# Optimization experiments

Measured on AMD Instinct MI355X. Metric: run time of the kernel, lower is better.

Reference implementation:

```python
import jax, jax.numpy as jnp
import numpy as np

N = 50000        # nodes
E = 600000       # edges
D_IN = 128       # node_in_channels
H = 256          # hidden_channels
G = 128          # graphs per batch
OUT = 1


def setup_inputs() -> dict:
    key = jax.random.key(0)
    ks = jax.random.split(key, 16)

    def lin(k, fan_in, fan_out):
        k1, k2 = jax.random.split(k)
        bound = 1.0 / np.sqrt(fan_in)
        W = jax.random.uniform(k1, (fan_in, fan_out), jnp.float32, -bound, bound)
        b = jax.random.uniform(k2, (fan_out,), jnp.float32, -bound, bound)
        return W, b

    x = jax.random.normal(ks[0], (N, D_IN), jnp.float32)
    edge_index = jax.random.randint(ks[1], (2, E), 0, N, jnp.int64)
    batch = jnp.sort(jax.random.randint(ks[2], (N,), 0, G, jnp.int64))

    W1, b1 = lin(ks[3], D_IN, H)   # conv1 mlp layer 1
    W2, b2 = lin(ks[4], H, H)      # conv1 mlp layer 2
    W3, b3 = lin(ks[5], H, H)      # conv2 mlp layer 1
    W4, b4 = lin(ks[6], H, H)      # conv2 mlp layer 2
    Wf1, bf1 = lin(ks[7], 2 * H, H)
    Wf2, bf2 = lin(ks[8], H, OUT)

    return {"x": x, "edge_index": edge_index, "batch": batch,
            "W1": W1, "b1": b1, "W2": W2, "b2": b2,
            "W3": W3, "b3": b3, "W4": W4, "b4": b4,
            "Wf1": Wf1, "bf1": bf1, "Wf2": Wf2, "bf2": bf2}


def _gin_conv(h, src, dst, Wa, ba, Wb, bb):
    # GINConv with eps=0: mlp(h + sum_{u->v} h[u])
    agg = jax.ops.segment_sum(h[src], dst, num_segments=h.shape[0])
    z = h + agg
    z = jax.nn.relu(z @ Wa + ba) @ Wb + bb
    return z


def reference(x, edge_index, batch,
              W1, b1, W2, b2, W3, b3, W4, b4,
              Wf1, bf1, Wf2, bf2):
    src, dst = edge_index[0], edge_index[1]

    h = jax.nn.relu(_gin_conv(x, src, dst, W1, b1, W2, b2))
    h = jax.nn.relu(_gin_conv(h, src, dst, W3, b3, W4, b4))

    # global mean / max pooling over graphs
    counts = jax.ops.segment_sum(jnp.ones((h.shape[0],), h.dtype), batch,
                                 num_segments=G)
    sums = jax.ops.segment_sum(h, batch, num_segments=G)
    mean = sums / jnp.maximum(counts, 1.0)[:, None]
    mx = jax.ops.segment_max(h, batch, num_segments=G)
    mx = jnp.where(counts[:, None] > 0, mx, 0.0)

    p = jnp.concatenate([mean, mx], axis=1)          # [G, 2H]
    out = jax.nn.relu(p @ Wf1 + bf1) @ Wf2 + bf2     # [G, OUT]
    return out
```

## Files before the change

### kernel.cpp

```cpp
#include <hip/hip_runtime.h>
#include <math.h>

#define D_IN 128
#define HDIM 256
#define PSPLIT 8

typedef __attribute__((ext_vector_type(8))) short bf16x8;
typedef __attribute__((ext_vector_type(4))) float f32x4;

__device__ inline ushort f2bf(float v) {
    union { float f; unsigned u; } c; c.f = v;
    unsigned u = c.u;
    return (ushort)((u + 0x7FFFu + ((u >> 16) & 1u)) >> 16);
}
__device__ inline float bf2f(ushort h) {
    union { unsigned u; float f; } c; c.u = ((unsigned)h) << 16; return c.f;
}
__device__ inline float bflo(unsigned u) {
    union { unsigned u; float f; } c; c.u = u << 16; return c.f;
}
__device__ inline float bfhi(unsigned u) {
    union { unsigned u; float f; } c; c.u = u & 0xFFFF0000u; return c.f;
}

__global__ __launch_bounds__(256) void zero_int_kernel(int* __restrict__ p, int n) {
    int i = blockIdx.x * 256 + threadIdx.x;
    int stride = gridDim.x * 256;
    for (; i < n; i += stride) p[i] = 0;
}

__global__ __launch_bounds__(256) void hist_kernel(
    const int* __restrict__ ei, int* __restrict__ deg, int E)
{
    int e = blockIdx.x * 256 + threadIdx.x;
    if (e < E) atomicAdd(&deg[ei[E + e]], 1);
}

__global__ __launch_bounds__(256) void scan_local_kernel(
    const int* __restrict__ deg, int* __restrict__ rowptr,
    int* __restrict__ bsum, int N)
{
    __shared__ int sh[256];
    const int t = threadIdx.x;
    const int i = blockIdx.x * 256 + t;
    int v = (i < N) ? deg[i] : 0;
    sh[t] = v;
    __syncthreads();
#pragma unroll
    for (int off = 1; off < 256; off <<= 1) {
        int x = (t >= off) ? sh[t - off] : 0;
        __syncthreads();
        sh[t] += x;
        __syncthreads();
    }
    if (i < N) rowptr[i] = sh[t] - v;
    if (t == 255) bsum[blockIdx.x] = sh[255];
}

__global__ __launch_bounds__(256) void scan_bsum_kernel(
    int* __restrict__ bsum, int* __restrict__ rowptr, int nb, int N)
{
    __shared__ int sh[256];
    const int t = threadIdx.x;
    int v = (t < nb) ? bsum[t] : 0;
    sh[t] = v;
    __syncthreads();
#pragma unroll
    for (int off = 1; off < 256; off <<= 1) {
        int x = (t >= off) ? sh[t - off] : 0;
        __syncthreads();
        sh[t] += x;
        __syncthreads();
    }
    if (t < nb) bsum[t] = sh[t] - v;
    if (t == 255) rowptr[N] = sh[255];
}

__global__ __launch_bounds__(256) void scan_apply_kernel(
    int* __restrict__ rowptr, int* __restrict__ cursor,
    const int* __restrict__ bsum, int N)
{
    int i = blockIdx.x * 256 + threadIdx.x;
    if (i < N) {
        int v = rowptr[i] + bsum[blockIdx.x];
        rowptr[i] = v;
        cursor[i] = v;
    }
}

__global__ __launch_bounds__(256) void fill_kernel(
    const int* __restrict__ ei, int* __restrict__ cursor,
    int* __restrict__ srclist, int E)
{
    int e = blockIdx.x * 256 + threadIdx.x;
    if (e < E) {
        int s = ei[e];
        int d = ei[E + e];
        int pos = atomicAdd(&cursor[d], 1);
        srclist[pos] = s;
    }
}

template<int K>
__global__ __launch_bounds__(256) void wsplit_kernel(
    const float* __restrict__ W, ushort* __restrict__ Wthi, ushort* __restrict__ Wtlo)
{
    int idx = blockIdx.x * 256 + threadIdx.x;
    if (idx >= K * 256) return;
    int k = idx >> 8;
    int c = idx & 255;
    float v = W[idx];
    ushort h = f2bf(v);
    Wthi[c * K + k] = h;
    Wtlo[c * K + k] = f2bf(v - bf2f(h));
}

__global__ __launch_bounds__(256) void gather1_kernel(
    const float* __restrict__ feat, const int* __restrict__ rowptr,
    const int* __restrict__ srclist, ushort* __restrict__ Zhi,
    ushort* __restrict__ Zlo, int N)
{
    const int wave = (blockIdx.x * 256 + threadIdx.x) >> 6;
    const int lane = threadIdx.x & 63;
    if (wave >= N) return;
    const int lo_ = rowptr[wave], hi_ = rowptr[wave + 1];
    const int c = lane * 2;
    float2 acc = *(const float2*)(feat + (size_t)wave * D_IN + c);
    int i = lo_;
    for (; i + 4 <= hi_; i += 4) {
        int s0 = srclist[i + 0], s1 = srclist[i + 1];
        int s2 = srclist[i + 2], s3 = srclist[i + 3];
        float2 v0 = *(const float2*)(feat + (size_t)s0 * D_IN + c);
        float2 v1 = *(const float2*)(feat + (size_t)s1 * D_IN + c);
        float2 v2 = *(const float2*)(feat + (size_t)s2 * D_IN + c);
        float2 v3 = *(const float2*)(feat + (size_t)s3 * D_IN + c);
        acc.x += v0.x + v1.x + v2.x + v3.x;
        acc.y += v0.y + v1.y + v2.y + v3.y;
    }
    for (; i < hi_; ++i) {
        int s = srclist[i];
        float2 v = *(const float2*)(feat + (size_t)s * D_IN + c);
        acc.x += v.x; acc.y += v.y;
    }
    ushort h0 = f2bf(acc.x), h1 = f2bf(acc.y);
    ushort l0 = f2bf(acc.x - bf2f(h0)), l1 = f2bf(acc.y - bf2f(h1));
    size_t o = ((size_t)wave * D_IN + c) >> 1;
    ((unsigned*)Zhi)[o] = (unsigned)h0 | ((unsigned)h1 << 16);
    ((unsigned*)Zlo)[o] = (unsigned)l0 | ((unsigned)l1 << 16);
}

__global__ __launch_bounds__(256) void gather2_kernel(
    const ushort* __restrict__ Fhi, const ushort* __restrict__ Flo,
    const int* __restrict__ rowptr, const int* __restrict__ srclist,
    ushort* __restrict__ Zhi, ushort* __restrict__ Zlo, int N)
{
    const int wave = (blockIdx.x * 256 + threadIdx.x) >> 6;
    const int lane = threadIdx.x & 63;
    if (wave >= N) return;
    const int lo_ = rowptr[wave], hi_ = rowptr[wave + 1];
    const int c = lane * 4;
    const size_t sbase = (size_t)wave * HDIM + c;
    uint2 sh = *(const uint2*)(Fhi + sbase);
    uint2 sl = *(const uint2*)(Flo + sbase);
    float a0 = bflo(sh.x) + bflo(sl.x);
    float a1 = bfhi(sh.x) + bfhi(sl.x);
    float a2 = bflo(sh.y) + bflo(sl.y);
    float a3 = bfhi(sh.y) + bfhi(sl.y);
    int i = lo_;
    for (; i + 2 <= hi_; i += 2) {
        int s0 = srclist[i], s1 = srclist[i + 1];
        uint2 h0 = *(const uint2*)(Fhi + (size_t)s0 * HDIM + c);
        uint2 l0 = *(const uint2*)(Flo + (size_t)s0 * HDIM + c);
        uint2 h1 = *(const uint2*)(Fhi + (size_t)s1 * HDIM + c);
        uint2 l1 = *(const uint2*)(Flo + (size_t)s1 * HDIM + c);
        a0 += bflo(h0.x) + bflo(l0.x) + bflo(h1.x) + bflo(l1.x);
        a1 += bfhi(h0.x) + bfhi(l0.x) + bfhi(h1.x) + bfhi(l1.x);
        a2 += bflo(h0.y) + bflo(l0.y) + bflo(h1.y) + bflo(l1.y);
        a3 += bfhi(h0.y) + bfhi(l0.y) + bfhi(h1.y) + bfhi(l1.y);
    }
    for (; i < hi_; ++i) {
        int s = srclist[i];
        uint2 vh = *(const uint2*)(Fhi + (size_t)s * HDIM + c);
        uint2 vl = *(const uint2*)(Flo + (size_t)s * HDIM + c);
        a0 += bflo(vh.x) + bflo(vl.x);
        a1 += bfhi(vh.x) + bfhi(vl.x);
        a2 += bflo(vh.y) + bflo(vl.y);
        a3 += bfhi(vh.y) + bfhi(vl.y);
    }
    ushort h0 = f2bf(a0), h1 = f2bf(a1), h2 = f2bf(a2), h3 = f2bf(a3);
    ushort l0 = f2bf(a0 - bf2f(h0)), l1 = f2bf(a1 - bf2f(h1));
    ushort l2 = f2bf(a2 - bf2f(h2)), l3 = f2bf(a3 - bf2f(h3));
    uint2 oh, ol;
    oh.x = (unsigned)h0 | ((unsigned)h1 << 16); oh.y = (unsigned)h2 | ((unsigned)h3 << 16);
    ol.x = (unsigned)l0 | ((unsigned)l1 << 16); ol.y = (unsigned)l2 | ((unsigned)l3 << 16);
    *(uint2*)(Zhi + sbase) = oh;
    *(uint2*)(Zlo + sbase) = ol;
}

template<int K, bool SPLIT_OUT>
__global__ __launch_bounds__(256) void mfma_gemm_kernel(
    const ushort* __restrict__ Ahi, const ushort* __restrict__ Alo,
    const ushort* __restrict__ Bthi, const ushort* __restrict__ Btlo,
    const float* __restrict__ Bias, float* __restrict__ OUTf,
    ushort* __restrict__ OUThi, ushort* __restrict__ OUTlo, int Nrows)
{
    __shared__ ushort As[2][64][40];
    __shared__ ushort Ws[2][256][40];
    const int t    = threadIdx.x;
    const int wv   = t >> 6;
    const int lane = t & 63;
    const int l15  = lane & 15;
    const int l4   = lane >> 4;
    const int row0 = blockIdx.x * 64;
    const int wc0  = wv * 64;

    f32x4 acc[4][4];
#pragma unroll
    for (int m = 0; m < 4; ++m)
#pragma unroll
        for (int n = 0; n < 4; ++n) acc[m][n] = (f32x4){0.f, 0.f, 0.f, 0.f};

    const int ar = t >> 2;
    const int as = (t & 3) * 8;
    const int grow = min(row0 + ar, Nrows - 1);
    const size_t abase = (size_t)grow * K + as;

    for (int k0 = 0; k0 < K; k0 += 32) {
        *(uint4*)&As[0][ar][as] = *(const uint4*)(Ahi + abase + k0);
        *(uint4*)&As[1][ar][as] = *(const uint4*)(Alo + abase + k0);
#pragma unroll
        for (int i = 0; i < 4; ++i) {
            int sid = t + i * 256;
            int wc  = sid >> 2;
            int wsg = (sid & 3) * 8;
            size_t wb = (size_t)wc * K + k0 + wsg;
            *(uint4*)&Ws[0][wc][wsg] = *(const uint4*)(Bthi + wb);
            *(uint4*)&Ws[1][wc][wsg] = *(const uint4*)(Btlo + wb);
        }
        __syncthreads();

        bf16x8 ah[4], al[4], bh[4], bl[4];
#pragma unroll
        for (int m = 0; m < 4; ++m) {
            ah[m] = *(const bf16x8*)&As[0][m * 16 + l15][l4 * 8];
            al[m] = *(const bf16x8*)&As[1][m * 16 + l15][l4 * 8];
        }
#pragma unroll
        for (int n = 0; n < 4; ++n) {
            bh[n] = *(const bf16x8*)&Ws[0][wc0 + n * 16 + l15][l4 * 8];
            bl[n] = *(const bf16x8*)&Ws[1][wc0 + n * 16 + l15][l4 * 8];
        }
#pragma unroll
        for (int m = 0; m < 4; ++m)
#pragma unroll
            for (int n = 0; n < 4; ++n) {
                acc[m][n] = __builtin_amdgcn_mfma_f32_16x16x32_bf16(ah[m], bh[n], acc[m][n], 0, 0, 0);
                acc[m][n] = __builtin_amdgcn_mfma_f32_16x16x32_bf16(ah[m], bl[n], acc[m][n], 0, 0, 0);
                acc[m][n] = __builtin_amdgcn_mfma_f32_16x16x32_bf16(al[m], bh[n], acc[m][n], 0, 0, 0);
            }
        __syncthreads();
    }

#pragma unroll
    for (int n = 0; n < 4; ++n) {
        const int ocol = wc0 + n * 16 + l15;
        const float bs = Bias[ocol];
#pragma unroll
        for (int m = 0; m < 4; ++m) {
#pragma unroll
            for (int r = 0; r < 4; ++r) {
                int orow = row0 + m * 16 + l4 * 4 + r;
                if (orow < Nrows) {
                    float v = fmaxf(acc[m][n][r] + bs, 0.f);
                    size_t o = (size_t)orow * HDIM + ocol;
                    if (SPLIT_OUT) {
                        ushort h = f2bf(v);
                        OUThi[o] = h;
                        OUTlo[o] = f2bf(v - bf2f(h));
                    } else {
                        OUTf[o] = v;
                    }
                }
            }
        }
    }
}

__global__ __launch_bounds__(256) void pool_partial_kernel(
    const float* __restrict__ h2, const int* __restrict__ batch,
    float* __restrict__ psum, float* __restrict__ pmax, int N)
{
    const int g = blockIdx.x / PSPLIT;
    const int s = blockIdx.x % PSPLIT;
    const int t = threadIdx.x;

    __shared__ int s_bounds[2];
    if (t < 2) {
        int target = g + t;
        int lo = 0, hi = N;
        while (lo < hi) {
            int mid = (lo + hi) >> 1;
            if (batch[mid] < target) lo = mid + 1; else hi = mid;
        }
        s_bounds[t] = lo;
    }
    __syncthreads();
    const int glo = s_bounds[0], ghi = s_bounds[1];
    const int cnt = ghi - glo;
    const int chunk = (cnt + PSPLIT - 1) / PSPLIT;
    const int clo = glo + s * chunk;
    const int chi = min(clo + chunk, ghi);

    float s0 = 0.f, s1 = 0.f, s2 = 0.f, s3 = 0.f;
    float m0 = -INFINITY, m1 = -INFINITY, m2 = -INFINITY, m3 = -INFINITY;
    int n = clo;
    for (; n + 4 <= chi; n += 4) {
        float v0 = h2[(size_t)(n + 0) * HDIM + t];
        float v1 = h2[(size_t)(n + 1) * HDIM + t];
        float v2 = h2[(size_t)(n + 2) * HDIM + t];
        float v3 = h2[(size_t)(n + 3) * HDIM + t];
        s0 += v0; m0 = fmaxf(m0, v0);
        s1 += v1; m1 = fmaxf(m1, v1);
        s2 += v2; m2 = fmaxf(m2, v2);
        s3 += v3; m3 = fmaxf(m3, v3);
    }
    for (; n < chi; ++n) {
        float v = h2[(size_t)n * HDIM + t];
        s0 += v; m0 = fmaxf(m0, v);
    }
    size_t o = (size_t)blockIdx.x * HDIM + t;
    psum[o] = (s0 + s1) + (s2 + s3);
    pmax[o] = fmaxf(fmaxf(m0, m1), fmaxf(m2, m3));
}

__global__ __launch_bounds__(256) void pool_final_kernel(
    const float* __restrict__ psum, const float* __restrict__ pmax,
    const int* __restrict__ batch,
    const float* __restrict__ Wf1, const float* __restrict__ bf1,
    const float* __restrict__ Wf2, const float* __restrict__ bf2,
    float* __restrict__ out, int N)
{
    const int g = blockIdx.x;
    const int t = threadIdx.x;

    __shared__ int s_bounds[2];
    if (t < 2) {
        int target = g + t;
        int lo = 0, hi = N;
        while (lo < hi) {
            int mid = (lo + hi) >> 1;
            if (batch[mid] < target) lo = mid + 1; else hi = mid;
        }
        s_bounds[t] = lo;
    }
    __syncthreads();
    const int cnt = s_bounds[1] - s_bounds[0];

    float sum = 0.f, mx = -INFINITY;
    const size_t gbase = (size_t)g * PSPLIT * HDIM + t;
#pragma unroll
    for (int s = 0; s < PSPLIT; ++s) {
        sum += psum[gbase + (size_t)s * HDIM];
        mx = fmaxf(mx, pmax[gbase + (size_t)s * HDIM]);
    }

    __shared__ float p[2 * HDIM];
    p[t]        = sum / (float)(cnt > 1 ? cnt : 1);
    p[HDIM + t] = (cnt > 0) ? mx : 0.f;
    __syncthreads();

    float acc = bf1[t];
#pragma unroll 8
    for (int k = 0; k < 2 * HDIM; ++k)
        acc += p[k] * Wf1[k * HDIM + t];
    float hval = fmaxf(acc, 0.f);

    float partial = hval * Wf2[t];
#pragma unroll
    for (int off = 32; off > 0; off >>= 1)
        partial += __shfl_down(partial, off);
    __shared__ float red[4];
    if ((t & 63) == 0) red[t >> 6] = partial;
    __syncthreads();
    if (t == 0) out[g] = red[0] + red[1] + red[2] + red[3] + bf2[0];
}

extern "C" void kernel_launch(void* const* d_in, const int* in_sizes, int n_in,
                              void* d_out, int out_size, void* d_ws, size_t ws_size,
                              hipStream_t stream)
{
    const float* x     = (const float*)d_in[0];
    const int*   ei    = (const int*)d_in[1];
    const int*   batch = (const int*)d_in[2];
    const float* W1 = (const float*)d_in[3];
    const float* b1 = (const float*)d_in[4];
    const float* W2 = (const float*)d_in[5];
    const float* b2 = (const float*)d_in[6];
    const float* W3 = (const float*)d_in[7];
    const float* b3 = (const float*)d_in[8];
    const float* W4 = (const float*)d_in[9];
    const float* b4 = (const float*)d_in[10];
    const float* Wf1 = (const float*)d_in[11];
    const float* bf1 = (const float*)d_in[12];
    const float* Wf2 = (const float*)d_in[13];
    const float* bf2 = (const float*)d_in[14];
    float* out = (float*)d_out;

    const int N  = in_sizes[0] / D_IN;
    const int E  = in_sizes[1] / 2;
    const int Gn = out_size;

    const size_t R = (size_t)N * HDIM;
    float* R0f = (float*)d_ws;
    float* R1f = R0f + R;
    ushort* R0u = (ushort*)R0f;
    ushort* R1u = (ushort*)R1f;

    ushort* wbuf = (ushort*)(R1f + R);
    ushort* W1thi = wbuf;
    ushort* W1tlo = W1thi + 128 * 256;
    ushort* W2thi = W1tlo + 128 * 256;
    ushort* W2tlo = W2thi + 256 * 256;
    ushort* W3thi = W2tlo + 256 * 256;
    ushort* W3tlo = W3thi + 256 * 256;
    ushort* W4thi = W3tlo + 256 * 256;
    ushort* W4tlo = W4thi + 256 * 256;

    int* rowptr  = (int*)(W4tlo + 256 * 256);
    int* cursor  = rowptr + (N + 1);
    int* srclist = cursor + N;
    float* psum  = (float*)(srclist + E);
    float* pmax  = psum + (size_t)Gn * PSPLIT * HDIM;
    int* bsum    = (int*)(pmax + (size_t)Gn * PSPLIT * HDIM);

    const int gblocks = (N + 63) / 64;
    const int eblocks = (E + 255) / 256;
    const int wblocks = (N + 3) / 4;
    const int nb      = (N + 255) / 256;

    zero_int_kernel<<<64, 256, 0, stream>>>(cursor, N);
    hist_kernel<<<eblocks, 256, 0, stream>>>(ei, cursor, E);
    scan_local_kernel<<<nb, 256, 0, stream>>>(cursor, rowptr, bsum, N);
    scan_bsum_kernel<<<1, 256, 0, stream>>>(bsum, rowptr, nb, N);
    scan_apply_kernel<<<nb, 256, 0, stream>>>(rowptr, cursor, bsum, N);
    fill_kernel<<<eblocks, 256, 0, stream>>>(ei, cursor, srclist, E);

    wsplit_kernel<128><<<128, 256, 0, stream>>>(W1, W1thi, W1tlo);
    wsplit_kernel<256><<<256, 256, 0, stream>>>(W2, W2thi, W2tlo);
    wsplit_kernel<256><<<256, 256, 0, stream>>>(W3, W3thi, W3tlo);
    wsplit_kernel<256><<<256, 256, 0, stream>>>(W4, W4thi, W4tlo);

    ushort* Z1hi = R0u;                 ushort* Z1lo = R0u + (size_t)N * D_IN;
    ushort* T1hi = R1u;                 ushort* T1lo = R1u + R;
    ushort* H1hi = R0u;                 ushort* H1lo = R0u + R;
    ushort* Z2hi = R1u;                 ushort* Z2lo = R1u + R;
    ushort* T2hi = R0u;                 ushort* T2lo = R0u + R;
    float*  H2   = R1f;

    gather1_kernel<<<wblocks, 256, 0, stream>>>(x, rowptr, srclist, Z1hi, Z1lo, N);
    mfma_gemm_kernel<128, true><<<gblocks, 256, 0, stream>>>(
        Z1hi, Z1lo, W1thi, W1tlo, b1, nullptr, T1hi, T1lo, N);
    mfma_gemm_kernel<256, true><<<gblocks, 256, 0, stream>>>(
        T1hi, T1lo, W2thi, W2tlo, b2, nullptr, H1hi, H1lo, N);

    gather2_kernel<<<wblocks, 256, 0, stream>>>(H1hi, H1lo, rowptr, srclist, Z2hi, Z2lo, N);
    mfma_gemm_kernel<256, true><<<gblocks, 256, 0, stream>>>(
        Z2hi, Z2lo, W3thi, W3tlo, b3, nullptr, T2hi, T2lo, N);
    mfma_gemm_kernel<256, false><<<gblocks, 256, 0, stream>>>(
        T2hi, T2lo, W4thi, W4tlo, b4, H2, nullptr, nullptr, N);

    pool_partial_kernel<<<Gn * PSPLIT, 256, 0, stream>>>(H2, batch, psum, pmax, N);
    pool_final_kernel<<<Gn, 256, 0, stream>>>(psum, pmax, batch,
                                              Wf1, bf1, Wf2, bf2, out, N);
}
```

Before: 540.5 us.

## Load GEMM tiles directly to LDS with swizzle; gather fp32 features with float4

The GEMM tile staging now uses global_load_lds, a direct global-to-LDS load, instead of going through registers. It drops the row padding and adds an XOR swizzle on the 16-byte chunks so the LDS reads still avoid bank conflicts. Gather1 now handles two nodes per wave with float4 loads. The second layer's GEMM now writes fp32 H1 instead of a bf16 hi/lo pair, so gather2 reads one fp32 float4 stream instead of two bf16 streams and needs no unpacking. This is meant to cut register traffic, LDS staging instructions and load instruction count in the gather. The trade-off is added correctness risk from the swizzle addressing and the per-wave LDS base layout of the direct loads.

```diff
diff --git a/kernel.cpp b/kernel.cpp
--- a/kernel.cpp
+++ b/kernel.cpp
@@ -7,6 +7,13 @@
 
 typedef __attribute__((ext_vector_type(8))) short bf16x8;
 typedef __attribute__((ext_vector_type(4))) float f32x4;
+
+#define GLOBAL_AS __attribute__((address_space(1)))
+#define LDS_AS    __attribute__((address_space(3)))
+
+__device__ __forceinline__ void gload16(const void* g, void* l) {
+    __builtin_amdgcn_global_load_lds((const GLOBAL_AS void*)g, (LDS_AS void*)l, 16, 0, 0);
+}
 
 __device__ inline ushort f2bf(float v) {
     union { float f; unsigned u; } c; c.f = v;
@@ -15,12 +22,6 @@
 }
 __device__ inline float bf2f(ushort h) {
     union { unsigned u; float f; } c; c.u = ((unsigned)h) << 16; return c.f;
-}
-__device__ inline float bflo(unsigned u) {
-    union { unsigned u; float f; } c; c.u = u << 16; return c.f;
-}
-__device__ inline float bfhi(unsigned u) {
-    union { unsigned u; float f; } c; c.u = u & 0xFFFF0000u; return c.f;
 }
 
 __global__ __launch_bounds__(256) void zero_int_kernel(int* __restrict__ p, int n) {
@@ -120,81 +121,80 @@
     const int* __restrict__ srclist, ushort* __restrict__ Zhi,
     ushort* __restrict__ Zlo, int N)
 {
-    const int wave = (blockIdx.x * 256 + threadIdx.x) >> 6;
+    const int wid  = (blockIdx.x * 256 + threadIdx.x) >> 6;
     const int lane = threadIdx.x & 63;
-    if (wave >= N) return;
-    const int lo_ = rowptr[wave], hi_ = rowptr[wave + 1];
-    const int c = lane * 2;
-    float2 acc = *(const float2*)(feat + (size_t)wave * D_IN + c);
+    const int node = wid * 2 + (lane >> 5);
+    if (node >= N) return;
+    const int lo_ = rowptr[node], hi_ = rowptr[node + 1];
+    const int c = (lane & 31) * 4;
+    float4 a = *(const float4*)(feat + (size_t)node * D_IN + c);
+    float s0 = a.x, s1 = a.y, s2 = a.z, s3 = a.w;
     int i = lo_;
     for (; i + 4 <= hi_; i += 4) {
-        int s0 = srclist[i + 0], s1 = srclist[i + 1];
-        int s2 = srclist[i + 2], s3 = srclist[i + 3];
-        float2 v0 = *(const float2*)(feat + (size_t)s0 * D_IN + c);
-        float2 v1 = *(const float2*)(feat + (size_t)s1 * D_IN + c);
-        float2 v2 = *(const float2*)(feat + (size_t)s2 * D_IN + c);
-        float2 v3 = *(const float2*)(feat + (size_t)s3 * D_IN + c);
-        acc.x += v0.x + v1.x + v2.x + v3.x;
-        acc.y += v0.y + v1.y + v2.y + v3.y;
+        int n0 = srclist[i], n1 = srclist[i + 1], n2 = srclist[i + 2], n3 = srclist[i + 3];
+        float4 v0 = *(const float4*)(feat + (size_t)n0 * D_IN + c);
+        float4 v1 = *(const float4*)(feat + (size_t)n1 * D_IN + c);
+        float4 v2 = *(const float4*)(feat + (size_t)n2 * D_IN + c);
+        float4 v3 = *(const float4*)(feat + (size_t)n3 * D_IN + c);
+        s0 += v0.x + v1.x + v2.x + v3.x;
+        s1 += v0.y + v1.y + v2.y + v3.y;
+        s2 += v0.z + v1.z + v2.z + v3.z;
+        s3 += v0.w + v1.w + v2.w + v3.w;
     }
     for (; i < hi_; ++i) {
         int s = srclist[i];
-        float2 v = *(const float2*)(feat + (size_t)s * D_IN + c);
-        acc.x += v.x; acc.y += v.y;
-    }
-    ushort h0 = f2bf(acc.x), h1 = f2bf(acc.y);
-    ushort l0 = f2bf(acc.x - bf2f(h0)), l1 = f2bf(acc.y - bf2f(h1));
-    size_t o = ((size_t)wave * D_IN + c) >> 1;
-    ((unsigned*)Zhi)[o] = (unsigned)h0 | ((unsigned)h1 << 16);
-    ((unsigned*)Zlo)[o] = (unsigned)l0 | ((unsigned)l1 << 16);
-}
-
-__global__ __launch_bounds__(256) void gather2_kernel(
-    const ushort* __restrict__ Fhi, const ushort* __restrict__ Flo,
-    const int* __restrict__ rowptr, const int* __restrict__ srclist,
-    ushort* __restrict__ Zhi, ushort* __restrict__ Zlo, int N)
-{
-    const int wave = (blockIdx.x * 256 + threadIdx.x) >> 6;
-    const int lane = threadIdx.x & 63;
-    if (wave >= N) return;
-    const int lo_ = rowptr[wave], hi_ = rowptr[wave + 1];
-    const int c = lane * 4;
-    const size_t sbase = (size_t)wave * HDIM + c;
-    uint2 sh = *(const uint2*)(Fhi + sbase);
-    uint2 sl = *(const uint2*)(Flo + sbase);
-    float a0 = bflo(sh.x) + bflo(sl.x);
-    float a1 = bfhi(sh.x) + bfhi(sl.x);
-    float a2 = bflo(sh.y) + bflo(sl.y);
-    float a3 = bfhi(sh.y) + bfhi(sl.y);
-    int i = lo_;
-    for (; i + 2 <= hi_; i += 2) {
-        int s0 = srclist[i], s1 = srclist[i + 1];
-        uint2 h0 = *(const uint2*)(Fhi + (size_t)s0 * HDIM + c);
-        uint2 l0 = *(const uint2*)(Flo + (size_t)s0 * HDIM + c);
-        uint2 h1 = *(const uint2*)(Fhi + (size_t)s1 * HDIM + c);
-        uint2 l1 = *(const uint2*)(Flo + (size_t)s1 * HDIM + c);
-        a0 += bflo(h0.x) + bflo(l0.x) + bflo(h1.x) + bflo(l1.x);
-        a1 += bfhi(h0.x) + bfhi(l0.x) + bfhi(h1.x) + bfhi(l1.x);
-        a2 += bflo(h0.y) + bflo(l0.y) + bflo(h1.y) + bflo(l1.y);
-        a3 += bfhi(h0.y) + bfhi(l0.y) + bfhi(h1.y) + bfhi(l1.y);
-    }
-    for (; i < hi_; ++i) {
-        int s = srclist[i];
-        uint2 vh = *(const uint2*)(Fhi + (size_t)s * HDIM + c);
-        uint2 vl = *(const uint2*)(Flo + (size_t)s * HDIM + c);
-        a0 += bflo(vh.x) + bflo(vl.x);
-        a1 += bfhi(vh.x) + bfhi(vl.x);
-        a2 += bflo(vh.y) + bflo(vl.y);
-        a3 += bfhi(vh.y) + bfhi(vl.y);
-    }
-    ushort h0 = f2bf(a0), h1 = f2bf(a1), h2 = f2bf(a2), h3 = f2bf(a3);
-    ushort l0 = f2bf(a0 - bf2f(h0)), l1 = f2bf(a1 - bf2f(h1));
-    ushort l2 = f2bf(a2 - bf2f(h2)), l3 = f2bf(a3 - bf2f(h3));
+        float4 v = *(const float4*)(feat + (size_t)s * D_IN + c);
+        s0 += v.x; s1 += v.y; s2 += v.z; s3 += v.w;
+    }
+    ushort h0 = f2bf(s0), h1 = f2bf(s1), h2 = f2bf(s2), h3 = f2bf(s3);
+    ushort l0 = f2bf(s0 - bf2f(h0)), l1 = f2bf(s1 - bf2f(h1));
+    ushort l2 = f2bf(s2 - bf2f(h2)), l3 = f2bf(s3 - bf2f(h3));
+    size_t o = (size_t)node * D_IN + c;
     uint2 oh, ol;
     oh.x = (unsigned)h0 | ((unsigned)h1 << 16); oh.y = (unsigned)h2 | ((unsigned)h3 << 16);
     ol.x = (unsigned)l0 | ((unsigned)l1 << 16); ol.y = (unsigned)l2 | ((unsigned)l3 << 16);
-    *(uint2*)(Zhi + sbase) = oh;
-    *(uint2*)(Zlo + sbase) = ol;
+    *(uint2*)(Zhi + o) = oh;
+    *(uint2*)(Zlo + o) = ol;
+}
+
+__global__ __launch_bounds__(256) void gather2_kernel(
+    const float* __restrict__ F, const int* __restrict__ rowptr,
+    const int* __restrict__ srclist,
+    ushort* __restrict__ Zhi, ushort* __restrict__ Zlo, int N)
+{
+    const int node = (blockIdx.x * 256 + threadIdx.x) >> 6;
+    const int lane = threadIdx.x & 63;
+    if (node >= N) return;
+    const int lo_ = rowptr[node], hi_ = rowptr[node + 1];
+    const int c = lane * 4;
+    float4 a = *(const float4*)(F + (size_t)node * HDIM + c);
+    float s0 = a.x, s1 = a.y, s2 = a.z, s3 = a.w;
+    int i = lo_;
+    for (; i + 4 <= hi_; i += 4) {
+        int n0 = srclist[i], n1 = srclist[i + 1], n2 = srclist[i + 2], n3 = srclist[i + 3];
+        float4 v0 = *(const float4*)(F + (size_t)n0 * HDIM + c);
+        float4 v1 = *(const float4*)(F + (size_t)n1 * HDIM + c);
+        float4 v2 = *(const float4*)(F + (size_t)n2 * HDIM + c);
+        float4 v3 = *(const float4*)(F + (size_t)n3 * HDIM + c);
+        s0 += v0.x + v1.x + v2.x + v3.x;
+        s1 += v0.y + v1.y + v2.y + v3.y;
+        s2 += v0.z + v1.z + v2.z + v3.z;
+        s3 += v0.w + v1.w + v2.w + v3.w;
+    }
+    for (; i < hi_; ++i) {
+        int s = srclist[i];
+        float4 v = *(const float4*)(F + (size_t)s * HDIM + c);
+        s0 += v.x; s1 += v.y; s2 += v.z; s3 += v.w;
+    }
+    ushort h0 = f2bf(s0), h1 = f2bf(s1), h2 = f2bf(s2), h3 = f2bf(s3);
+    ushort l0 = f2bf(s0 - bf2f(h0)), l1 = f2bf(s1 - bf2f(h1));
+    ushort l2 = f2bf(s2 - bf2f(h2)), l3 = f2bf(s3 - bf2f(h3));
+    size_t o = (size_t)node * HDIM + c;
+    uint2 oh, ol;
+    oh.x = (unsigned)h0 | ((unsigned)h1 << 16); oh.y = (unsigned)h2 | ((unsigned)h3 << 16);
+    ol.x = (unsigned)l0 | ((unsigned)l1 << 16); ol.y = (unsigned)l2 | ((unsigned)l3 << 16);
+    *(uint2*)(Zhi + o) = oh;
+    *(uint2*)(Zlo + o) = ol;
 }
 
 template<int K, bool SPLIT_OUT>
@@ -204,8 +204,8 @@
     const float* __restrict__ Bias, float* __restrict__ OUTf,
     ushort* __restrict__ OUThi, ushort* __restrict__ OUTlo, int Nrows)
 {
-    __shared__ ushort As[2][64][40];
-    __shared__ ushort Ws[2][256][40];
+    __shared__ ushort As[2][64][32];
+    __shared__ ushort Ws[2][256][32];
     const int t    = threadIdx.x;
     const int wv   = t >> 6;
     const int lane = t & 63;
@@ -214,41 +214,41 @@
     const int row0 = blockIdx.x * 64;
     const int wc0  = wv * 64;
 
+    const int srow   = lane >> 2;
+    const int schunk = (lane & 3) ^ ((lane >> 3) & 3);
+    const int rchunk = (l4 ^ ((l15 >> 1) & 3)) * 8;
+
     f32x4 acc[4][4];
 #pragma unroll
     for (int m = 0; m < 4; ++m)
 #pragma unroll
         for (int n = 0; n < 4; ++n) acc[m][n] = (f32x4){0.f, 0.f, 0.f, 0.f};
 
-    const int ar = t >> 2;
-    const int as = (t & 3) * 8;
-    const int grow = min(row0 + ar, Nrows - 1);
-    const size_t abase = (size_t)grow * K + as;
+    const int agrow = min(row0 + wv * 16 + srow, Nrows - 1);
+    const size_t abase = (size_t)agrow * K + schunk * 8;
 
     for (int k0 = 0; k0 < K; k0 += 32) {
-        *(uint4*)&As[0][ar][as] = *(const uint4*)(Ahi + abase + k0);
-        *(uint4*)&As[1][ar][as] = *(const uint4*)(Alo + abase + k0);
-#pragma unroll
-        for (int i = 0; i < 4; ++i) {
-            int sid = t + i * 256;
-            int wc  = sid >> 2;
-            int wsg = (sid & 3) * 8;
-            size_t wb = (size_t)wc * K + k0 + wsg;
-            *(uint4*)&Ws[0][wc][wsg] = *(const uint4*)(Bthi + wb);
-            *(uint4*)&Ws[1][wc][wsg] = *(const uint4*)(Btlo + wb);
-        }
+#pragma unroll
+        for (int j = 0; j < 4; ++j) {
+            const int g = wv * 4 + j;
+            const size_t wb = (size_t)(g * 16 + srow) * K + k0 + schunk * 8;
+            gload16(Bthi + wb, &Ws[0][g * 16][0]);
+            gload16(Btlo + wb, &Ws[1][g * 16][0]);
+        }
+        gload16(Ahi + abase + k0, &As[0][wv * 16][0]);
+        gload16(Alo + abase + k0, &As[1][wv * 16][0]);
         __syncthreads();
 
         bf16x8 ah[4], al[4], bh[4], bl[4];
 #pragma unroll
         for (int m = 0; m < 4; ++m) {
-            ah[m] = *(const bf16x8*)&As[0][m * 16 + l15][l4 * 8];
-            al[m] = *(const bf16x8*)&As[1][m * 16 + l15][l4 * 8];
+            ah[m] = *(const bf16x8*)&As[0][m * 16 + l15][rchunk];
+            al[m] = *(const bf16x8*)&As[1][m * 16 + l15][rchunk];
         }
 #pragma unroll
         for (int n = 0; n < 4; ++n) {
-            bh[n] = *(const bf16x8*)&Ws[0][wc0 + n * 16 + l15][l4 * 8];
-            bl[n] = *(const bf16x8*)&Ws[1][wc0 + n * 16 + l15][l4 * 8];
+            bh[n] = *(const bf16x8*)&Ws[0][wc0 + n * 16 + l15][rchunk];
+            bl[n] = *(const bf16x8*)&Ws[1][wc0 + n * 16 + l15][rchunk];
         }
 #pragma unroll
         for (int m = 0; m < 4; ++m)
@@ -433,10 +433,11 @@
     float* pmax  = psum + (size_t)Gn * PSPLIT * HDIM;
     int* bsum    = (int*)(pmax + (size_t)Gn * PSPLIT * HDIM);
 
-    const int gblocks = (N + 63) / 64;
-    const int eblocks = (E + 255) / 256;
-    const int wblocks = (N + 3) / 4;
-    const int nb      = (N + 255) / 256;
+    const int gblocks  = (N + 63) / 64;
+    const int eblocks  = (E + 255) / 256;
+    const int wblocks2 = (N + 3) / 4;
+    const int wblocks1 = ((N + 1) / 2 + 3) / 4;
+    const int nb       = (N + 255) / 256;
 
     zero_int_kernel<<<64, 256, 0, stream>>>(cursor, N);
     hist_kernel<<<eblocks, 256, 0, stream>>>(ei, cursor, E);
@@ -452,18 +453,18 @@
 
     ushort* Z1hi = R0u;                 ushort* Z1lo = R0u + (size_t)N * D_IN;
     ushort* T1hi = R1u;                 ushort* T1lo = R1u + R;
-    ushort* H1hi = R0u;                 ushort* H1lo = R0u + R;
+    float*  H1   = R0f;
     ushort* Z2hi = R1u;                 ushort* Z2lo = R1u + R;
     ushort* T2hi = R0u;                 ushort* T2lo = R0u + R;
     float*  H2   = R1f;
 
-    gather1_kernel<<<wblocks, 256, 0, stream>>>(x, rowptr, srclist, Z1hi, Z1lo, N);
+    gather1_kernel<<<wblocks1, 256, 0, stream>>>(x, rowptr, srclist, Z1hi, Z1lo, N);
     mfma_gemm_kernel<128, true><<<gblocks, 256, 0, stream>>>(
         Z1hi, Z1lo, W1thi, W1tlo, b1, nullptr, T1hi, T1lo, N);
-    mfma_gemm_kernel<256, true><<<gblocks, 256, 0, stream>>>(
-        T1hi, T1lo, W2thi, W2tlo, b2, nullptr, H1hi, H1lo, N);
-
-    gather2_kernel<<<wblocks, 256, 0, stream>>>(H1hi, H1lo, rowptr, srclist, Z2hi, Z2lo, N);
+    mfma_gemm_kernel<256, false><<<gblocks, 256, 0, stream>>>(
+        T1hi, T1lo, W2thi, W2tlo, b2, H1, nullptr, nullptr, N);
+
+    gather2_kernel<<<wblocks2, 256, 0, stream>>>(H1, rowptr, srclist, Z2hi, Z2lo, N);
     mfma_gemm_kernel<256, true><<<gblocks, 256, 0, stream>>>(
         Z2hi, Z2lo, W3thi, W3tlo, b3, nullptr, T2hi, T2lo, N);
     mfma_gemm_kernel<256, false><<<gblocks, 256, 0, stream>>>(
```

New measurement: 523.3 us. 1.03x faster.
